# Kernel optimization log

Measured on AMD Instinct MI355X. Metric: run time of the kernel, lower is better.

The kernel has to match this reference:

```python
import jax, jax.numpy as jnp
import numpy as np

BZ, N_STEPS, D_IN, D_HID, D_OUT = 4096, 128, 32, 128, 32


def setup_inputs() -> dict:
    key = jax.random.key(0)
    ks = jax.random.split(key, 16)
    g = lambda k, s: jax.random.normal(k, s, dtype=jnp.float32) * 0.05
    return {
        "fcn_latent": g(ks[0], (BZ, D_IN)),
        "encoder_outputs": g(ks[1], (BZ, N_STEPS, D_HID)),
        "att1_w": g(ks[2], (D_IN, 2 * D_IN)),
        "att1_b": g(ks[3], (D_IN,)),
        "att2_w": g(ks[4], (D_HID, 2 * D_HID)),
        "att2_b": g(ks[5], (D_HID,)),
        "gru1_wih": g(ks[6], (3 * D_HID, D_IN)),
        "gru1_whh": g(ks[7], (3 * D_HID, D_HID)),
        "gru1_bih": g(ks[8], (3 * D_HID,)),
        "gru1_bhh": g(ks[9], (3 * D_HID,)),
        "gru2_wih": g(ks[10], (3 * D_HID, D_HID)),
        "gru2_whh": g(ks[11], (3 * D_HID, D_HID)),
        "gru2_bih": g(ks[12], (3 * D_HID,)),
        "gru2_bhh": g(ks[13], (3 * D_HID,)),
        "out_w": g(ks[14], (D_OUT, D_HID)),
        "out_b": g(ks[15], (D_OUT,)),
    }


def _gru_cell(x, h, w_ih, w_hh, b_ih, b_hh):
    # torch.nn.GRUCell math: gates ordered (r, z, n)
    gi = x @ w_ih.T + b_ih
    gh = h @ w_hh.T + b_hh
    i_r, i_z, i_n = jnp.split(gi, 3, axis=-1)
    h_r, h_z, h_n = jnp.split(gh, 3, axis=-1)
    r = jax.nn.sigmoid(i_r + h_r)
    z = jax.nn.sigmoid(i_z + h_z)
    n = jnp.tanh(i_n + r * h_n)
    return (1.0 - z) * n + z * h


def _attend(h, enc_t, w, b):
    # h: (bz, D), enc_t: (bz, d_enc). Faithful to original (mixes batch into contraction).
    scores = h.T @ enc_t                     # (D, d_enc)
    weight = jax.nn.softmax(scores, axis=-1)
    context = (weight @ enc_t.T).T           # (bz, D)
    return jnp.tanh(jnp.concatenate([context, h], axis=1) @ w.T + b)


def reference(fcn_latent, encoder_outputs, att1_w, att1_b, att2_w, att2_b,
              gru1_wih, gru1_whh, gru1_bih, gru1_bhh,
              gru2_wih, gru2_whh, gru2_bih, gru2_bhh, out_w, out_b):
    # step 0: attention over d_input-sized hidden, then GRUCell(d_input -> d_hidden)
    att0 = _attend(fcn_latent, encoder_outputs[:, 0, :], att1_w, att1_b)
    h_rep = jnp.tile(fcn_latent, (1, D_HID // D_IN))          # (bz, d_hidden)
    h = _gru_cell(att0, h_rep, gru1_wih, gru1_whh, gru1_bih, gru1_bhh)

    def step(h, enc_t):
        a = _attend(h, enc_t, att2_w, att2_b)
        h2 = _gru_cell(a, h, gru2_wih, gru2_whh, gru2_bih, gru2_bhh)
        return h2, h2

    enc_rest = jnp.swapaxes(encoder_outputs[:, 1:, :], 0, 1)  # (n_steps-1, bz, d_hidden)
    _, hs_rest = jax.lax.scan(step, h, enc_rest)
    collector = jnp.concatenate([h[:, None, :], jnp.swapaxes(hs_rest, 0, 1)], axis=1)
    reconstruction = collector @ out_w.T + out_b              # (bz, n_steps, d_output)
    return reconstruction
```

## Files before the change

### kernel.cpp

```cpp
#include <hip/hip_runtime.h>
#include <math.h>

#define BZ 4096
#define NT 128
#define DH 128
#define DI 32
#define LDW 132
#define SCR_KS 2116
#define SA 136
#define ST 40

typedef short bf16x8 __attribute__((ext_vector_type(8)));
typedef float f32x4 __attribute__((ext_vector_type(4)));

__device__ __forceinline__ float4 ld4(const float* p) { return *(const float4*)(p); }
__device__ __forceinline__ void st4(float* p, float4 v) { *(float4*)(p) = v; }
__device__ __forceinline__ float dot4(float4 w, float4 a) {
  return w.x*a.x + w.y*a.y + w.z*a.z + w.w*a.w;
}
__device__ __forceinline__ float sigm(float x) { return 1.f / (1.f + expf(-x)); }
__device__ __forceinline__ unsigned short f2b(float x) {
  unsigned u = __float_as_uint(x);
  u += 0x7FFFu + ((u >> 16) & 1u);
  return (unsigned short)(u >> 16);
}

__global__ __launch_bounds__(512) void k_prep(const float* __restrict__ a2w,
                                              const float* __restrict__ wih,
                                              const float* __restrict__ whh,
                                              const float* __restrict__ outw,
                                              unsigned short* __restrict__ wbf) {
  const int idx = blockIdx.x * 512 + threadIdx.x;
  if (idx >= 147456) return;
  const int tile = idx >> 14, pos = idx & 16383;
  float v;
  if (tile == 0)      v = a2w[(pos >> 7) * 256 + (pos & 127)];
  else if (tile == 1) v = a2w[(pos >> 7) * 256 + 128 + (pos & 127)];
  else if (tile == 2) v = wih[pos];
  else if (tile == 3) v = whh[pos];
  else if (tile == 4) v = wih[16384 + pos];
  else if (tile == 5) v = whh[16384 + pos];
  else if (tile == 6) v = wih[32768 + pos];
  else if (tile == 7) v = whh[32768 + pos];
  else                v = (pos < 4096) ? outw[pos] : 0.f;
  wbf[idx] = f2b(v);
}

template<int D>
__global__ __launch_bounds__(512) void k_scores(const float* __restrict__ hsrc,
                                                const float* __restrict__ enc,
                                                int t, float* __restrict__ spart) {
  constexpr int IG = D / 8;
  constexpr int JC = (D == 128) ? 4 : 1;
  constexpr int HS = D + 4;
  __shared__ float hs[64 * HS];
  __shared__ float es[64 * LDW];
  const int p = blockIdx.x, tid = threadIdx.x, b0 = p * 64;
  for (int idx = tid; idx < 64 * (D / 4); idx += 512) {
    const int r = idx / (D / 4), c4 = (idx % (D / 4)) * 4;
    st4(hs + r * HS + c4, ld4(hsrc + (size_t)(b0 + r) * D + c4));
  }
  for (int idx = tid; idx < 64 * 32; idx += 512) {
    const int r = idx >> 5, c4 = (idx & 31) << 2;
    st4(es + r * LDW + c4, ld4(enc + ((size_t)(b0 + r) * NT + t) * DH + c4));
  }
  __syncthreads();
  const int ig = tid % IG, jg = tid / IG;
  const int i0 = ig * 8, j0 = jg * JC;
  float acc[8][JC];
#pragma unroll
  for (int a = 0; a < 8; ++a)
#pragma unroll
    for (int b = 0; b < JC; ++b) acc[a][b] = 0.f;
  for (int b = 0; b < 64; ++b) {
    float4 h0 = ld4(hs + b * HS + i0);
    float4 h1 = ld4(hs + b * HS + i0 + 4);
    float hv[8] = {h0.x, h0.y, h0.z, h0.w, h1.x, h1.y, h1.z, h1.w};
    float ev[JC];
    if (JC == 4) {
      float4 e = ld4(es + b * LDW + j0);
      ev[0] = e.x; ev[1] = e.y; ev[2] = e.z; ev[3] = e.w;
    } else {
      ev[0] = es[b * LDW + j0];
    }
#pragma unroll
    for (int ii = 0; ii < 8; ++ii)
#pragma unroll
      for (int jj = 0; jj < JC; ++jj) acc[ii][jj] += hv[ii] * ev[jj];
  }
#pragma unroll
  for (int ii = 0; ii < 8; ++ii)
#pragma unroll
    for (int jj = 0; jj < JC; ++jj)
      spart[((size_t)p * D + (i0 + ii)) * 128 + j0 + jj] = acc[ii][jj];
}

template<int R, int P>
__global__ __launch_bounds__(128) void k_soft(const float* __restrict__ spart,
                                              float* __restrict__ W,
                                              unsigned short* __restrict__ Wmb) {
  const int r = blockIdx.x, j = threadIdx.x;
  float s = 0.f;
#pragma unroll 8
  for (int p = 0; p < P; ++p) s += spart[((size_t)p * R + r) * 128 + j];
  __shared__ float xm[2], xs[2];
  float m = s;
  for (int o = 1; o < 64; o <<= 1) m = fmaxf(m, __shfl_xor(m, o));
  if ((j & 63) == 0) xm[j >> 6] = m;
  __syncthreads();
  m = fmaxf(xm[0], xm[1]);
  float e = expf(s - m);
  float sum = e;
  for (int o = 1; o < 64; o <<= 1) sum += __shfl_xor(sum, o);
  if ((j & 63) == 0) xs[j >> 6] = sum;
  __syncthreads();
  sum = xs[0] + xs[1];
  const float val = e / sum;
  W[r * 128 + j] = val;
  Wmb[r * 128 + j] = f2b(val);
}

__global__ __launch_bounds__(128) void k_sum(const float* __restrict__ spart,
                                             float* __restrict__ S1,
                                             float* __restrict__ S2) {
  const int r = blockIdx.x, j = threadIdx.x;
  float s = 0.f;
#pragma unroll 8
  for (int p = 0; p < 64; ++p) s += spart[((size_t)p * 128 + r) * 128 + j];
  S1[r * 128 + j] = s;
  S2[r * 128 + j] = 0.f;
}

struct WTile { bf16x8 k[4]; };
struct AFrag { bf16x8 k[4]; };

__device__ __forceinline__ void loadW(WTile& wt, const unsigned short* __restrict__ base,
                                      int R, int g) {
#pragma unroll
  for (int ks = 0; ks < 4; ++ks)
    wt.k[ks] = *(const bf16x8*)(base + (size_t)R * 128 + ks * 32 + g * 8);
}
__device__ __forceinline__ void loadA(AFrag& a, const unsigned short* act, int n, int g) {
  const char* ab = (const char*)act + n * (2 * SA) + g * 16;
#pragma unroll
  for (int ks = 0; ks < 4; ++ks) a.k[ks] = *(const bf16x8*)(ab + ks * 64);
}
__device__ __forceinline__ void mmrr(f32x4& acc, const AFrag& a, const WTile& w) {
#pragma unroll
  for (int ks = 0; ks < 4; ++ks)
    acc = __builtin_amdgcn_mfma_f32_16x16x32_bf16(a.k[ks], w.k[ks], acc, 0, 0, 0);
}
__device__ __forceinline__ void mmls(f32x4& acc, const unsigned short* Wt,
                                     const unsigned short* act, int R, int n, int g) {
  const char* ab = (const char*)act + n * (2 * SA) + g * 16;
  const char* wb = (const char*)Wt;
  const int sw = (R & 7) << 4;
#pragma unroll
  for (int ks = 0; ks < 4; ++ks) {
    bf16x8 b = *(const bf16x8*)(wb + ((R * 256 + ks * 64 + g * 16) ^ sw));
    bf16x8 a = *(const bf16x8*)(ab + ks * 64);
    acc = __builtin_amdgcn_mfma_f32_16x16x32_bf16(a, b, acc, 0, 0, 0);
  }
}

__global__ __launch_bounds__(512, 2) void k_step3(
    const float* __restrict__ enc, int t, int do_next,
    const float* __restrict__ Srd, float* __restrict__ Sac, float* __restrict__ Szr,
    const unsigned short* __restrict__ wbf,
    const float* __restrict__ att2b,
    const float* __restrict__ bih, const float* __restrict__ bhh,
    const float* __restrict__ outb,
    float* __restrict__ h, float* __restrict__ out) {
  __shared__ __align__(16) unsigned short Wslot[16384];
  __shared__ __align__(16) unsigned short el[32 * SA], hl[32 * SA];
  __shared__ __align__(16) unsigned short ctxl[32 * SA], al[32 * SA], hnl[32 * SA];
  __shared__ __align__(16) unsigned short hnT[128 * ST], encT[128 * ST];
  const int tid = threadIdx.x, b0 = blockIdx.x * 32;
  const int w = tid >> 6, l = tid & 63;
  const int n = l & 15, g4 = l >> 4;
  const int c = w * 16 + n;
  const f32x4 z4 = {0.f, 0.f, 0.f, 0.f};

  {
    const int row = tid >> 2, q = tid & 3;
    const float* sr = Srd + row * 128 + q * 32;
    float4 v[8];
    float mx = -1e30f;
#pragma unroll
    for (int i = 0; i < 8; ++i) {
      v[i] = ld4(sr + 4 * i);
      mx = fmaxf(mx, fmaxf(fmaxf(v[i].x, v[i].y), fmaxf(v[i].z, v[i].w)));
    }
    mx = fmaxf(mx, __shfl_xor(mx, 1));
    mx = fmaxf(mx, __shfl_xor(mx, 2));
    float sum = 0.f;
#pragma unroll
    for (int i = 0; i < 8; ++i) {
      v[i].x = expf(v[i].x - mx); v[i].y = expf(v[i].y - mx);
      v[i].z = expf(v[i].z - mx); v[i].w = expf(v[i].w - mx);
      sum += (v[i].x + v[i].y) + (v[i].z + v[i].w);
    }
    sum += __shfl_xor(sum, 1);
    sum += __shfl_xor(sum, 2);
    const float inv = 1.f / sum;
    char* wb = (char*)Wslot;
    const int sw = (row & 7) << 4;
#pragma unroll
    for (int ch = 0; ch < 4; ++ch) {
      unsigned short h8[8] = {
        f2b(v[2*ch].x * inv),   f2b(v[2*ch].y * inv),
        f2b(v[2*ch].z * inv),   f2b(v[2*ch].w * inv),
        f2b(v[2*ch+1].x * inv), f2b(v[2*ch+1].y * inv),
        f2b(v[2*ch+1].z * inv), f2b(v[2*ch+1].w * inv)
      };
      *(uint4*)(wb + ((row * 256 + q * 64 + ch * 16) ^ sw)) = *(const uint4*)h8;
    }
  }

  {
    const int r = tid >> 4, c8 = (tid & 15) << 3;
    float4 e0 = ld4(enc + ((size_t)(b0 + r) * NT + t) * DH + c8);
    float4 e1 = ld4(enc + ((size_t)(b0 + r) * NT + t) * DH + c8 + 4);
    float4 h0 = ld4(h + (size_t)(b0 + r) * DH + c8);
    float4 h1 = ld4(h + (size_t)(b0 + r) * DH + c8 + 4);
    unsigned short e8[8] = {f2b(e0.x), f2b(e0.y), f2b(e0.z), f2b(e0.w),
                            f2b(e1.x), f2b(e1.y), f2b(e1.z), f2b(e1.w)};
    unsigned short h8[8] = {f2b(h0.x), f2b(h0.y), f2b(h0.z), f2b(h0.w),
                            f2b(h1.x), f2b(h1.y), f2b(h1.z), f2b(h1.w)};
    *(uint4*)(el + r * SA + c8) = *(const uint4*)e8;
    *(uint4*)(hl + r * SA + c8) = *(const uint4*)h8;
  }
  if (do_next) {
    const int r = tid & 31, c8 = (tid >> 5) << 3;
    float4 e0 = ld4(enc + ((size_t)(b0 + r) * NT + t + 1) * DH + c8);
    float4 e1 = ld4(enc + ((size_t)(b0 + r) * NT + t + 1) * DH + c8 + 4);
    encT[(c8 + 0) * ST + r] = f2b(e0.x); encT[(c8 + 1) * ST + r] = f2b(e0.y);
    encT[(c8 + 2) * ST + r] = f2b(e0.z); encT[(c8 + 3) * ST + r] = f2b(e0.w);
    encT[(c8 + 4) * ST + r] = f2b(e1.x); encT[(c8 + 5) * ST + r] = f2b(e1.y);
    encT[(c8 + 6) * ST + r] = f2b(e1.z); encT[(c8 + 7) * ST + r] = f2b(e1.w);
  }
  if (do_next && tid < 128) Szr[blockIdx.x * 128 + tid] = 0.f;

  WTile wA2a, wA2b, wIR, wHR, wIZ, wHZ, wIN, wHN;
  loadW(wA2a, wbf + 0 * 16384, c, g4);
  loadW(wA2b, wbf + 1 * 16384, c, g4);
  loadW(wIR,  wbf + 2 * 16384, c, g4);
  loadW(wHR,  wbf + 3 * 16384, c, g4);
  loadW(wIZ,  wbf + 4 * 16384, c, g4);
  loadW(wHZ,  wbf + 5 * 16384, c, g4);
  loadW(wIN,  wbf + 6 * 16384, c, g4);
  loadW(wHN,  wbf + 7 * 16384, c, g4);

  float hprev[2][4];
#pragma unroll
  for (int hh = 0; hh < 2; ++hh)
#pragma unroll
    for (int j = 0; j < 4; ++j)
      hprev[hh][j] = h[(size_t)(b0 + hh * 16 + g4 * 4 + j) * DH + c];
  const float b2c = att2b[c];
  const float bihR = bih[c], bihZ = bih[DH + c], bihN = bih[2 * DH + c];
  const float bhhR = bhh[c], bhhZ = bhh[DH + c], bhhN = bhh[2 * DH + c];
  __syncthreads();

#pragma unroll
  for (int hh = 0; hh < 2; ++hh) {
    f32x4 aC = z4;
    mmls(aC, Wslot, el + hh * 16 * SA, c, n, g4);
#pragma unroll
    for (int j = 0; j < 4; ++j) ctxl[(hh * 16 + g4 * 4 + j) * SA + c] = f2b(aC[j]);
  }
  __syncthreads();
#pragma unroll
  for (int hh = 0; hh < 2; ++hh) {
    AFrag fC, fH;
    loadA(fC, ctxl + hh * 16 * SA, n, g4);
    loadA(fH, hl + hh * 16 * SA, n, g4);
    f32x4 aA = z4;
    mmrr(aA, fC, wA2a);
    mmrr(aA, fH, wA2b);
#pragma unroll
    for (int j = 0; j < 4; ++j)
      al[(hh * 16 + g4 * 4 + j) * SA + c] = f2b(tanhf(aA[j] + b2c));
  }
  __syncthreads();
  f32x4 aR[2], aZ[2], aIN[2], aHN[2];
#pragma unroll
  for (int hh = 0; hh < 2; ++hh) {
    AFrag fA, fH;
    loadA(fA, al + hh * 16 * SA, n, g4);
    loadA(fH, hl + hh * 16 * SA, n, g4);
    f32x4 tr_ = z4, tz = z4, ti = z4, th = z4;
    mmrr(tr_, fA, wIR); mmrr(tr_, fH, wHR);
    mmrr(tz, fA, wIZ);  mmrr(tz, fH, wHZ);
    mmrr(ti, fA, wIN);  mmrr(th, fH, wHN);
    aR[hh] = tr_; aZ[hh] = tz; aIN[hh] = ti; aHN[hh] = th;
  }
#pragma unroll
  for (int hh = 0; hh < 2; ++hh) {
#pragma unroll
    for (int j = 0; j < 4; ++j) {
      const int row = hh * 16 + g4 * 4 + j;
      const float rg = sigm(aR[hh][j] + bihR + bhhR);
      const float zg = sigm(aZ[hh][j] + bihZ + bhhZ);
      const float ng = tanhf(aIN[hh][j] + bihN + rg * (aHN[hh][j] + bhhN));
      const float hv = (1.f - zg) * ng + zg * hprev[hh][j];
      const unsigned short hb = f2b(hv);
      hnl[row * SA + c] = hb;
      hnT[c * ST + row] = hb;
      h[(size_t)(b0 + row) * DH + c] = hv;
    }
  }
  __syncthreads();
  if (w < 2) {
    WTile wOut;
    loadW(wOut, wbf + 8 * 16384, c, g4);
    const float ob = outb[c];
#pragma unroll
    for (int hh = 0; hh < 2; ++hh) {
      AFrag fO;
      loadA(fO, hnl + hh * 16 * SA, n, g4);
      f32x4 o = z4;
      mmrr(o, fO, wOut);
#pragma unroll
      for (int j = 0; j < 4; ++j)
        out[((size_t)(b0 + hh * 16 + g4 * 4 + j) * NT + t) * DI + c] = o[j] + ob;
    }
  }
  if (do_next) {
    bf16x8 afr = *(const bf16x8*)(hnT + (16 * w + n) * ST + g4 * 8);
    float* Sn = Sac + (size_t)(16 * w + g4 * 4) * 128 + n;
#pragma unroll
    for (int nt = 0; nt < 8; ++nt) {
      bf16x8 bfr = *(const bf16x8*)(encT + (16 * nt + n) * ST + g4 * 8);
      f32x4 s = __builtin_amdgcn_mfma_f32_16x16x32_bf16(afr, bfr, z4, 0, 0, 0);
#pragma unroll
      for (int jj = 0; jj < 4; ++jj) atomicAdd(Sn + jj * 128 + nt * 16, s[jj]);
    }
  }
}

__device__ __forceinline__ void stage128(float* dst, const float* __restrict__ src,
                                         int rows, int srcStride, int tid) {
  const int n4 = rows * 32;
  for (int idx = tid; idx < n4; idx += 512) {
    const int r = idx >> 5, c4 = (idx & 31) << 2;
    st4(dst + r * LDW + c4, ld4(src + (size_t)r * srcStride + c4));
  }
}
template<int ADD>
__device__ __forceinline__ void phase128(float* Wb, const float* act, float* dest, int tid) {
  const int ks = tid & 7, cg_ = (tid >> 3) & 15, r4 = tid >> 7;
  const int rbase = r4 * 4;
  float acc[4][8];
#pragma unroll
  for (int a = 0; a < 4; ++a)
#pragma unroll
    for (int b = 0; b < 8; ++b) acc[a][b] = 0.f;
#pragma unroll
  for (int ch = 0; ch < 4; ++ch) {
    const int k = ks * 4 + ch * 32;
    float4 av[4];
#pragma unroll
    for (int ri = 0; ri < 4; ++ri) av[ri] = ld4(act + (rbase + ri) * LDW + k);
#pragma unroll
    for (int i = 0; i < 8; ++i) {
      float4 wv = ld4(Wb + (cg_ * 8 + i) * LDW + k);
#pragma unroll
      for (int ri = 0; ri < 4; ++ri) acc[ri][i] += dot4(wv, av[ri]);
    }
  }
  __syncthreads();
#pragma unroll
  for (int ri = 0; ri < 4; ++ri) {
    st4(Wb + ks * SCR_KS + (rbase + ri) * LDW + cg_ * 8,
        make_float4(acc[ri][0], acc[ri][1], acc[ri][2], acc[ri][3]));
    st4(Wb + ks * SCR_KS + (rbase + ri) * LDW + cg_ * 8 + 4,
        make_float4(acc[ri][4], acc[ri][5], acc[ri][6], acc[ri][7]));
  }
  __syncthreads();
  const int fr = tid >> 5, fc = (tid & 31) << 2;
  float4 s = make_float4(0.f, 0.f, 0.f, 0.f);
#pragma unroll
  for (int kk = 0; kk < 8; ++kk) {
    float4 v = ld4(Wb + kk * SCR_KS + fr * LDW + fc);
    s.x += v.x; s.y += v.y; s.z += v.z; s.w += v.w;
  }
  float* dp = dest + fr * LDW + fc;
  if (ADD) { float4 o = ld4(dp); s.x += o.x; s.y += o.y; s.z += o.z; s.w += o.w; }
  st4(dp, s);
  __syncthreads();
}
__device__ __forceinline__ void gru_out(float p0, float p1, float p2, float p3,
                                        float bi0, float bi1, float bi2,
                                        float bh0, float bh1, float bh2,
                                        float hv, float* o) {
  const float rg = sigm(p0 + bi0 + bh0);
  const float zg = sigm(p1 + bi1 + bh1);
  const float ng = tanhf(p2 + bi2 + rg * (p3 + bh2));
  *o = (1.f - zg) * ng + zg * hv;
}
__global__ __launch_bounds__(512) void k_main0(
    const float* __restrict__ enc, const float* __restrict__ fcn,
    const float* __restrict__ W0,
    const float* __restrict__ A1, const float* __restrict__ b1,
    const float* __restrict__ wih, const float* __restrict__ whh,
    const float* __restrict__ bih, const float* __restrict__ bhh,
    const float* __restrict__ outw, const float* __restrict__ outb,
    float* __restrict__ h, float* __restrict__ out) {
  __shared__ float Wb[16960];
  __shared__ float el[16 * LDW], hrep[16 * LDW], al[16 * LDW], hn[16 * LDW];
  __shared__ float pre[4][16 * LDW];
  __shared__ float fl[16 * 36];
  const int tid = threadIdx.x, b0 = blockIdx.x * 16;
  {
    const int r = tid >> 5, c4 = (tid & 31) << 2;
    st4(el + r * LDW + c4, ld4(enc + ((size_t)(b0 + r) * NT + 0) * DH + c4));
  }
  {
    const int r = tid >> 5, cc = tid & 31;
    fl[r * 36 + cc] = fcn[(size_t)(b0 + r) * DI + cc];
  }
  __syncthreads();
  {
    const int r = tid >> 5, fc = (tid & 31) << 2;
    st4(hrep + r * LDW + fc, ld4(fl + r * 36 + (fc & 31)));
  }
  stage128(Wb, W0, 32, 128, tid);
  __syncthreads();
  {
    const int r = tid >> 5, q = tid & 31;
    float acc = 0.f;
#pragma unroll 8
    for (int k4 = 0; k4 < 32; ++k4)
      acc += dot4(ld4(Wb + q * LDW + k4 * 4), ld4(el + r * LDW + k4 * 4));
    hn[r * LDW + q] = acc;
  }
  __syncthreads();
  for (int idx = tid; idx < 512; idx += 512) {
    const int r = idx >> 4, c4 = (idx & 15) << 2;
    st4(Wb + r * 68 + c4, ld4(A1 + r * 64 + c4));
  }
  __syncthreads();
  {
    const int r = tid >> 5, i = tid & 31;
    float acc = b1[i];
#pragma unroll
    for (int k4 = 0; k4 < 8; ++k4)
      acc += dot4(ld4(Wb + i * 68 + k4 * 4), ld4(hn + r * LDW + k4 * 4));
#pragma unroll
    for (int k4 = 0; k4 < 8; ++k4)
      acc += dot4(ld4(Wb + i * 68 + 32 + k4 * 4), ld4(fl + r * 36 + k4 * 4));
    al[r * LDW + i] = tanhf(acc);
  }
  __syncthreads();
  for (int idx = tid; idx < 384 * 8; idx += 512) {
    const int r = idx >> 3, c4 = (idx & 7) << 2;
    st4(Wb + r * 36 + c4, ld4(wih + r * 32 + c4));
  }
  __syncthreads();
  {
    const int r = tid >> 5, ccc = tid & 31;
#pragma unroll
    for (int m = 0; m < 12; ++m) {
      const int cc = ccc + 32 * m, g = cc >> 7, col = cc & 127;
      float acc = 0.f;
#pragma unroll
      for (int k4 = 0; k4 < 8; ++k4)
        acc += dot4(ld4(Wb + cc * 36 + k4 * 4), ld4(al + r * LDW + k4 * 4));
      pre[(g == 2) ? 2 : g][r * LDW + col] = acc;
    }
  }
  __syncthreads();
  stage128(Wb, whh, 128, 128, tid);          __syncthreads();
  phase128<1>(Wb, hrep, pre[0], tid);
  stage128(Wb, whh + 16384, 128, 128, tid);  __syncthreads();
  phase128<1>(Wb, hrep, pre[1], tid);
  stage128(Wb, whh + 32768, 128, 128, tid);  __syncthreads();
  phase128<0>(Wb, hrep, pre[3], tid);
  {
    const int fr = tid >> 5, fc = (tid & 31) << 2;
    float4 p0 = ld4(&pre[0][fr * LDW + fc]), p1 = ld4(&pre[1][fr * LDW + fc]);
    float4 p2 = ld4(&pre[2][fr * LDW + fc]), p3 = ld4(&pre[3][fr * LDW + fc]);
    float4 bi0 = ld4(bih + fc), bi1 = ld4(bih + DH + fc), bi2 = ld4(bih + 2 * DH + fc);
    float4 bh0 = ld4(bhh + fc), bh1 = ld4(bhh + DH + fc), bh2 = ld4(bhh + 2 * DH + fc);
    float4 hv = ld4(hrep + fr * LDW + fc);
    float o0, o1, o2, o3;
    gru_out(p0.x, p1.x, p2.x, p3.x, bi0.x, bi1.x, bi2.x, bh0.x, bh1.x, bh2.x, hv.x, &o0);
    gru_out(p0.y, p1.y, p2.y, p3.y, bi0.y, bi1.y, bi2.y, bh0.y, bh1.y, bh2.y, hv.y, &o1);
    gru_out(p0.z, p1.z, p2.z, p3.z, bi0.z, bi1.z, bi2.z, bh0.z, bh1.z, bh2.z, hv.z, &o2);
    gru_out(p0.w, p1.w, p2.w, p3.w, bi0.w, bi1.w, bi2.w, bh0.w, bh1.w, bh2.w, hv.w, &o3);
    float4 hnew = make_float4(o0, o1, o2, o3);
    st4(hn + fr * LDW + fc, hnew);
    st4(h + (size_t)(b0 + fr) * DH + fc, hnew);
  }
  __syncthreads();
  stage128(Wb, outw, 32, 128, tid);
  __syncthreads();
  {
    const int r = tid >> 5, cc = tid & 31;
    float acc = outb[cc];
#pragma unroll 8
    for (int k4 = 0; k4 < 32; ++k4)
      acc += dot4(ld4(Wb + cc * LDW + k4 * 4), ld4(hn + r * LDW + k4 * 4));
    out[((size_t)(b0 + r) * NT + 0) * DI + cc] = acc;
  }
}

extern "C" void kernel_launch(void* const* d_in, const int* in_sizes, int n_in,
                              void* d_out, int out_size, void* d_ws, size_t ws_size,
                              hipStream_t stream) {
  (void)in_sizes; (void)n_in; (void)out_size; (void)ws_size;
  const float* fcn  = (const float*)d_in[0];
  const float* enc  = (const float*)d_in[1];
  const float* a1w  = (const float*)d_in[2];
  const float* a1b  = (const float*)d_in[3];
  const float* a2w  = (const float*)d_in[4];
  const float* a2b  = (const float*)d_in[5];
  const float* w1ih = (const float*)d_in[6];
  const float* w1hh = (const float*)d_in[7];
  const float* b1ih = (const float*)d_in[8];
  const float* b1hh = (const float*)d_in[9];
  const float* w2ih = (const float*)d_in[10];
  const float* w2hh = (const float*)d_in[11];
  const float* b2ih = (const float*)d_in[12];
  const float* b2hh = (const float*)d_in[13];
  const float* outw = (const float*)d_in[14];
  const float* outb = (const float*)d_in[15];
  float* out = (float*)d_out;
  float* ws  = (float*)d_ws;

  float* h     = ws;
  float* spart = ws + 524288;
  float* Wbuf  = ws + 1572864;
  float* Sbuf  = ws + 1589248;
  unsigned short* wbf = (unsigned short*)(ws + 1654784);
  unsigned short* Wmb = (unsigned short*)(ws + 1728512);

  k_prep<<<288, 512, 0, stream>>>(a2w, w2ih, w2hh, outw, wbf);

  k_scores<DI><<<64, 512, 0, stream>>>(fcn, enc, 0, spart);
  k_soft<DI, 64><<<DI, 128, 0, stream>>>(spart, Wbuf, Wmb);
  k_main0<<<BZ / 16, 512, 0, stream>>>(enc, fcn, Wbuf, a1w, a1b,
                                       w1ih, w1hh, b1ih, b1hh, outw, outb, h, out);
  k_scores<DH><<<64, 512, 0, stream>>>(h, enc, 1, spart);
  k_sum<<<128, 128, 0, stream>>>(spart, Sbuf + 16384, Sbuf + 2 * 16384);

  for (int t = 1; t < NT; ++t) {
    const int do_next = (t < NT - 1) ? 1 : 0;
    const float* Srd = Sbuf + (size_t)(t & 3) * 16384;
    float* Sac = Sbuf + (size_t)((t + 1) & 3) * 16384;
    float* Szr = Sbuf + (size_t)((t + 2) & 3) * 16384;
    k_step3<<<128, 512, 0, stream>>>(enc, t, do_next, Srd, Sac, Szr, wbf, a2b,
                                     b2ih, b2hh, outb, h, out);
  }
}
```

Measured before the change: 3.242 ms.

## Halve per-block batch rows and keep softmax weights in registers

```diff
diff --git a/kernel.cpp b/kernel.cpp
--- a/kernel.cpp
+++ b/kernel.cpp
@@ -8,7 +8,7 @@
 #define LDW 132
 #define SCR_KS 2116
 #define SA 136
-#define ST 40
+#define ST2 48
 
 typedef short bf16x8 __attribute__((ext_vector_type(8)));
 typedef float f32x4 __attribute__((ext_vector_type(4)));
@@ -150,20 +150,8 @@
   for (int ks = 0; ks < 4; ++ks)
     acc = __builtin_amdgcn_mfma_f32_16x16x32_bf16(a.k[ks], w.k[ks], acc, 0, 0, 0);
 }
-__device__ __forceinline__ void mmls(f32x4& acc, const unsigned short* Wt,
-                                     const unsigned short* act, int R, int n, int g) {
-  const char* ab = (const char*)act + n * (2 * SA) + g * 16;
-  const char* wb = (const char*)Wt;
-  const int sw = (R & 7) << 4;
-#pragma unroll
-  for (int ks = 0; ks < 4; ++ks) {
-    bf16x8 b = *(const bf16x8*)(wb + ((R * 256 + ks * 64 + g * 16) ^ sw));
-    bf16x8 a = *(const bf16x8*)(ab + ks * 64);
-    acc = __builtin_amdgcn_mfma_f32_16x16x32_bf16(a, b, acc, 0, 0, 0);
-  }
-}
-
-__global__ __launch_bounds__(512, 2) void k_step3(
+
+__global__ __launch_bounds__(512, 2) void k_step4(
     const float* __restrict__ enc, int t, int do_next,
     const float* __restrict__ Srd, float* __restrict__ Sac, float* __restrict__ Szr,
     const unsigned short* __restrict__ wbf,
@@ -171,28 +159,29 @@
     const float* __restrict__ bih, const float* __restrict__ bhh,
     const float* __restrict__ outb,
     float* __restrict__ h, float* __restrict__ out) {
-  __shared__ __align__(16) unsigned short Wslot[16384];
-  __shared__ __align__(16) unsigned short el[32 * SA], hl[32 * SA];
-  __shared__ __align__(16) unsigned short ctxl[32 * SA], al[32 * SA], hnl[32 * SA];
-  __shared__ __align__(16) unsigned short hnT[128 * ST], encT[128 * ST];
-  const int tid = threadIdx.x, b0 = blockIdx.x * 32;
+  __shared__ __align__(16) unsigned short el[16 * SA], hl[16 * SA];
+  __shared__ __align__(16) unsigned short ctxl[16 * SA], al[16 * SA], hnl[16 * SA];
+  __shared__ __align__(16) unsigned short hnT[128 * ST2], encT[128 * ST2];
+  const int tid = threadIdx.x, b0 = blockIdx.x * 16;
   const int w = tid >> 6, l = tid & 63;
   const int n = l & 15, g4 = l >> 4;
   const int c = w * 16 + n;
   const f32x4 z4 = {0.f, 0.f, 0.f, 0.f};
 
-  {
-    const int row = tid >> 2, q = tid & 3;
-    const float* sr = Srd + row * 128 + q * 32;
+  WTile wW;
+  {
+    const float* sr = Srd + c * 128 + g4 * 8;
     float4 v[8];
     float mx = -1e30f;
 #pragma unroll
-    for (int i = 0; i < 8; ++i) {
-      v[i] = ld4(sr + 4 * i);
-      mx = fmaxf(mx, fmaxf(fmaxf(v[i].x, v[i].y), fmaxf(v[i].z, v[i].w)));
-    }
-    mx = fmaxf(mx, __shfl_xor(mx, 1));
-    mx = fmaxf(mx, __shfl_xor(mx, 2));
+    for (int ks = 0; ks < 4; ++ks) {
+      v[2 * ks]     = ld4(sr + ks * 32);
+      v[2 * ks + 1] = ld4(sr + ks * 32 + 4);
+      mx = fmaxf(mx, fmaxf(fmaxf(v[2*ks].x, v[2*ks].y), fmaxf(v[2*ks].z, v[2*ks].w)));
+      mx = fmaxf(mx, fmaxf(fmaxf(v[2*ks+1].x, v[2*ks+1].y), fmaxf(v[2*ks+1].z, v[2*ks+1].w)));
+    }
+    mx = fmaxf(mx, __shfl_xor(mx, 16));
+    mx = fmaxf(mx, __shfl_xor(mx, 32));
     float sum = 0.f;
 #pragma unroll
     for (int i = 0; i < 8; ++i) {
@@ -200,24 +189,22 @@
       v[i].z = expf(v[i].z - mx); v[i].w = expf(v[i].w - mx);
       sum += (v[i].x + v[i].y) + (v[i].z + v[i].w);
     }
-    sum += __shfl_xor(sum, 1);
-    sum += __shfl_xor(sum, 2);
+    sum += __shfl_xor(sum, 16);
+    sum += __shfl_xor(sum, 32);
     const float inv = 1.f / sum;
-    char* wb = (char*)Wslot;
-    const int sw = (row & 7) << 4;
-#pragma unroll
-    for (int ch = 0; ch < 4; ++ch) {
+#pragma unroll
+    for (int ks = 0; ks < 4; ++ks) {
       unsigned short h8[8] = {
-        f2b(v[2*ch].x * inv),   f2b(v[2*ch].y * inv),
-        f2b(v[2*ch].z * inv),   f2b(v[2*ch].w * inv),
-        f2b(v[2*ch+1].x * inv), f2b(v[2*ch+1].y * inv),
-        f2b(v[2*ch+1].z * inv), f2b(v[2*ch+1].w * inv)
+        f2b(v[2*ks].x * inv),   f2b(v[2*ks].y * inv),
+        f2b(v[2*ks].z * inv),   f2b(v[2*ks].w * inv),
+        f2b(v[2*ks+1].x * inv), f2b(v[2*ks+1].y * inv),
+        f2b(v[2*ks+1].z * inv), f2b(v[2*ks+1].w * inv)
       };
-      *(uint4*)(wb + ((row * 256 + q * 64 + ch * 16) ^ sw)) = *(const uint4*)h8;
-    }
-  }
-
-  {
+      wW.k[ks] = *(const bf16x8*)h8;
+    }
+  }
+
+  if (tid < 256) {
     const int r = tid >> 4, c8 = (tid & 15) << 3;
     float4 e0 = ld4(enc + ((size_t)(b0 + r) * NT + t) * DH + c8);
     float4 e1 = ld4(enc + ((size_t)(b0 + r) * NT + t) * DH + c8 + 4);
@@ -229,109 +216,103 @@
                             f2b(h1.x), f2b(h1.y), f2b(h1.z), f2b(h1.w)};
     *(uint4*)(el + r * SA + c8) = *(const uint4*)e8;
     *(uint4*)(hl + r * SA + c8) = *(const uint4*)h8;
-  }
-  if (do_next) {
-    const int r = tid & 31, c8 = (tid >> 5) << 3;
+  } else if (do_next) {
+    const int idx = tid - 256;
+    const int r = idx & 15, c8 = (idx >> 4) << 3;
     float4 e0 = ld4(enc + ((size_t)(b0 + r) * NT + t + 1) * DH + c8);
     float4 e1 = ld4(enc + ((size_t)(b0 + r) * NT + t + 1) * DH + c8 + 4);
-    encT[(c8 + 0) * ST + r] = f2b(e0.x); encT[(c8 + 1) * ST + r] = f2b(e0.y);
-    encT[(c8 + 2) * ST + r] = f2b(e0.z); encT[(c8 + 3) * ST + r] = f2b(e0.w);
-    encT[(c8 + 4) * ST + r] = f2b(e1.x); encT[(c8 + 5) * ST + r] = f2b(e1.y);
-    encT[(c8 + 6) * ST + r] = f2b(e1.z); encT[(c8 + 7) * ST + r] = f2b(e1.w);
-  }
-  if (do_next && tid < 128) Szr[blockIdx.x * 128 + tid] = 0.f;
-
-  WTile wA2a, wA2b, wIR, wHR, wIZ, wHZ, wIN, wHN;
-  loadW(wA2a, wbf + 0 * 16384, c, g4);
-  loadW(wA2b, wbf + 1 * 16384, c, g4);
-  loadW(wIR,  wbf + 2 * 16384, c, g4);
-  loadW(wHR,  wbf + 3 * 16384, c, g4);
-  loadW(wIZ,  wbf + 4 * 16384, c, g4);
-  loadW(wHZ,  wbf + 5 * 16384, c, g4);
-  loadW(wIN,  wbf + 6 * 16384, c, g4);
-  loadW(wHN,  wbf + 7 * 16384, c, g4);
-
-  float hprev[2][4];
-#pragma unroll
-  for (int hh = 0; hh < 2; ++hh)
-#pragma unroll
-    for (int j = 0; j < 4; ++j)
-      hprev[hh][j] = h[(size_t)(b0 + hh * 16 + g4 * 4 + j) * DH + c];
+    encT[(c8 + 0) * ST2 + r] = f2b(e0.x); encT[(c8 + 1) * ST2 + r] = f2b(e0.y);
+    encT[(c8 + 2) * ST2 + r] = f2b(e0.z); encT[(c8 + 3) * ST2 + r] = f2b(e0.w);
+    encT[(c8 + 4) * ST2 + r] = f2b(e1.x); encT[(c8 + 5) * ST2 + r] = f2b(e1.y);
+    encT[(c8 + 6) * ST2 + r] = f2b(e1.z); encT[(c8 + 7) * ST2 + r] = f2b(e1.w);
+  }
+  if (do_next) {
+    for (int q = tid; q < 128 * 32; q += 512) {
+      const int col = q >> 5, p = q & 31;
+      hnT[col * ST2 + 16 + p] = 0;
+      encT[col * ST2 + 16 + p] = 0;
+    }
+    if (tid < 64) Szr[blockIdx.x * 64 + tid] = 0.f;
+  }
+
+  float hprev[4];
+#pragma unroll
+  for (int j = 0; j < 4; ++j)
+    hprev[j] = h[(size_t)(b0 + g4 * 4 + j) * DH + c];
   const float b2c = att2b[c];
   const float bihR = bih[c], bihZ = bih[DH + c], bihN = bih[2 * DH + c];
   const float bhhR = bhh[c], bhhZ = bhh[DH + c], bhhN = bhh[2 * DH + c];
-  __syncthreads();
-
-#pragma unroll
-  for (int hh = 0; hh < 2; ++hh) {
+
+  WTile wA, wB;
+  loadW(wA, wbf + 0 * 16384, c, g4);
+  loadW(wB, wbf + 1 * 16384, c, g4);
+  __syncthreads();
+
+  {
+    AFrag fE;
+    loadA(fE, el, n, g4);
     f32x4 aC = z4;
-    mmls(aC, Wslot, el + hh * 16 * SA, c, n, g4);
-#pragma unroll
-    for (int j = 0; j < 4; ++j) ctxl[(hh * 16 + g4 * 4 + j) * SA + c] = f2b(aC[j]);
-  }
-  __syncthreads();
-#pragma unroll
-  for (int hh = 0; hh < 2; ++hh) {
-    AFrag fC, fH;
-    loadA(fC, ctxl + hh * 16 * SA, n, g4);
-    loadA(fH, hl + hh * 16 * SA, n, g4);
+    mmrr(aC, fE, wW);
+#pragma unroll
+    for (int j = 0; j < 4; ++j) ctxl[(g4 * 4 + j) * SA + c] = f2b(aC[j]);
+  }
+  __syncthreads();
+  AFrag fH;
+  loadA(fH, hl, n, g4);
+  {
+    AFrag fC;
+    loadA(fC, ctxl, n, g4);
     f32x4 aA = z4;
-    mmrr(aA, fC, wA2a);
-    mmrr(aA, fH, wA2b);
+    mmrr(aA, fC, wA);
+    mmrr(aA, fH, wB);
 #pragma unroll
     for (int j = 0; j < 4; ++j)
-      al[(hh * 16 + g4 * 4 + j) * SA + c] = f2b(tanhf(aA[j] + b2c));
-  }
-  __syncthreads();
-  f32x4 aR[2], aZ[2], aIN[2], aHN[2];
-#pragma unroll
-  for (int hh = 0; hh < 2; ++hh) {
-    AFrag fA, fH;
-    loadA(fA, al + hh * 16 * SA, n, g4);
-    loadA(fH, hl + hh * 16 * SA, n, g4);
-    f32x4 tr_ = z4, tz = z4, ti = z4, th = z4;
-    mmrr(tr_, fA, wIR); mmrr(tr_, fH, wHR);
-    mmrr(tz, fA, wIZ);  mmrr(tz, fH, wHZ);
-    mmrr(ti, fA, wIN);  mmrr(th, fH, wHN);
-    aR[hh] = tr_; aZ[hh] = tz; aIN[hh] = ti; aHN[hh] = th;
-  }
-#pragma unroll
-  for (int hh = 0; hh < 2; ++hh) {
-#pragma unroll
-    for (int j = 0; j < 4; ++j) {
-      const int row = hh * 16 + g4 * 4 + j;
-      const float rg = sigm(aR[hh][j] + bihR + bhhR);
-      const float zg = sigm(aZ[hh][j] + bihZ + bhhZ);
-      const float ng = tanhf(aIN[hh][j] + bihN + rg * (aHN[hh][j] + bhhN));
-      const float hv = (1.f - zg) * ng + zg * hprev[hh][j];
-      const unsigned short hb = f2b(hv);
-      hnl[row * SA + c] = hb;
-      hnT[c * ST + row] = hb;
-      h[(size_t)(b0 + row) * DH + c] = hv;
-    }
+      al[(g4 * 4 + j) * SA + c] = f2b(tanhf(aA[j] + b2c));
+  }
+  loadW(wA, wbf + 2 * 16384, c, g4);
+  loadW(wB, wbf + 3 * 16384, c, g4);
+  __syncthreads();
+  AFrag fA;
+  loadA(fA, al, n, g4);
+  f32x4 aR = z4, aZ = z4, aIN = z4, aHN = z4;
+  mmrr(aR, fA, wA); mmrr(aR, fH, wB);
+  loadW(wA, wbf + 4 * 16384, c, g4);
+  loadW(wB, wbf + 5 * 16384, c, g4);
+  mmrr(aZ, fA, wA); mmrr(aZ, fH, wB);
+  loadW(wA, wbf + 6 * 16384, c, g4);
+  loadW(wB, wbf + 7 * 16384, c, g4);
+  mmrr(aIN, fA, wA); mmrr(aHN, fH, wB);
+#pragma unroll
+  for (int j = 0; j < 4; ++j) {
+    const int row = g4 * 4 + j;
+    const float rg = sigm(aR[j] + bihR + bhhR);
+    const float zg = sigm(aZ[j] + bihZ + bhhZ);
+    const float ng = tanhf(aIN[j] + bihN + rg * (aHN[j] + bhhN));
+    const float hv = (1.f - zg) * ng + zg * hprev[j];
+    const unsigned short hb = f2b(hv);
+    hnl[row * SA + c] = hb;
+    hnT[c * ST2 + row] = hb;
+    h[(size_t)(b0 + row) * DH + c] = hv;
   }
   __syncthreads();
   if (w < 2) {
     WTile wOut;
     loadW(wOut, wbf + 8 * 16384, c, g4);
+    AFrag fO;
+    loadA(fO, hnl, n, g4);
+    f32x4 o = z4;
+    mmrr(o, fO, wOut);
     const float ob = outb[c];
 #pragma unroll
-    for (int hh = 0; hh < 2; ++hh) {
-      AFrag fO;
-      loadA(fO, hnl + hh * 16 * SA, n, g4);
-      f32x4 o = z4;
-      mmrr(o, fO, wOut);
-#pragma unroll
-      for (int j = 0; j < 4; ++j)
-        out[((size_t)(b0 + hh * 16 + g4 * 4 + j) * NT + t) * DI + c] = o[j] + ob;
-    }
+    for (int j = 0; j < 4; ++j)
+      out[((size_t)(b0 + g4 * 4 + j) * NT + t) * DI + c] = o[j] + ob;
   }
   if (do_next) {
-    bf16x8 afr = *(const bf16x8*)(hnT + (16 * w + n) * ST + g4 * 8);
+    bf16x8 afr = *(const bf16x8*)(hnT + (16 * w + n) * ST2 + g4 * 8);
     float* Sn = Sac + (size_t)(16 * w + g4 * 4) * 128 + n;
 #pragma unroll
     for (int nt = 0; nt < 8; ++nt) {
-      bf16x8 bfr = *(const bf16x8*)(encT + (16 * nt + n) * ST + g4 * 8);
+      bf16x8 bfr = *(const bf16x8*)(encT + (16 * nt + n) * ST2 + g4 * 8);
       f32x4 s = __builtin_amdgcn_mfma_f32_16x16x32_bf16(afr, bfr, z4, 0, 0, 0);
 #pragma unroll
       for (int jj = 0; jj < 4; ++jj) atomicAdd(Sn + jj * 128 + nt * 16, s[jj]);
@@ -550,7 +531,7 @@
     const float* Srd = Sbuf + (size_t)(t & 3) * 16384;
     float* Sac = Sbuf + (size_t)((t + 1) & 3) * 16384;
     float* Szr = Sbuf + (size_t)((t + 2) & 3) * 16384;
-    k_step3<<<128, 512, 0, stream>>>(enc, t, do_next, Srd, Sac, Szr, wbf, a2b,
+    k_step4<<<256, 512, 0, stream>>>(enc, t, do_next, Srd, Sac, Szr, wbf, a2b,
                                      b2ih, b2hh, outb, h, out);
   }
 }
```

Result: slower. 4.099 ms (+26.5%).

## Defer output projection to a batched kernel over stored hidden-state history

Applied to the files above, without the earlier changes.

```diff
diff --git a/kernel.cpp b/kernel.cpp
--- a/kernel.cpp
+++ b/kernel.cpp
@@ -169,17 +169,18 @@
     const unsigned short* __restrict__ wbf,
     const float* __restrict__ att2b,
     const float* __restrict__ bih, const float* __restrict__ bhh,
-    const float* __restrict__ outb,
-    float* __restrict__ h, float* __restrict__ out) {
+    float* __restrict__ hist) {
   __shared__ __align__(16) unsigned short Wslot[16384];
   __shared__ __align__(16) unsigned short el[32 * SA], hl[32 * SA];
-  __shared__ __align__(16) unsigned short ctxl[32 * SA], al[32 * SA], hnl[32 * SA];
+  __shared__ __align__(16) unsigned short ctxl[32 * SA], al[32 * SA];
   __shared__ __align__(16) unsigned short hnT[128 * ST], encT[128 * ST];
   const int tid = threadIdx.x, b0 = blockIdx.x * 32;
   const int w = tid >> 6, l = tid & 63;
   const int n = l & 15, g4 = l >> 4;
   const int c = w * 16 + n;
   const f32x4 z4 = {0.f, 0.f, 0.f, 0.f};
+  const float* __restrict__ hprev_g = hist + (size_t)(t - 1) * (BZ * DH);
+  float* __restrict__ hcur_g = hist + (size_t)t * (BZ * DH);
 
   {
     const int row = tid >> 2, q = tid & 3;
@@ -221,8 +222,8 @@
     const int r = tid >> 4, c8 = (tid & 15) << 3;
     float4 e0 = ld4(enc + ((size_t)(b0 + r) * NT + t) * DH + c8);
     float4 e1 = ld4(enc + ((size_t)(b0 + r) * NT + t) * DH + c8 + 4);
-    float4 h0 = ld4(h + (size_t)(b0 + r) * DH + c8);
-    float4 h1 = ld4(h + (size_t)(b0 + r) * DH + c8 + 4);
+    float4 h0 = ld4(hprev_g + (size_t)(b0 + r) * DH + c8);
+    float4 h1 = ld4(hprev_g + (size_t)(b0 + r) * DH + c8 + 4);
     unsigned short e8[8] = {f2b(e0.x), f2b(e0.y), f2b(e0.z), f2b(e0.w),
                             f2b(e1.x), f2b(e1.y), f2b(e1.z), f2b(e1.w)};
     unsigned short h8[8] = {f2b(h0.x), f2b(h0.y), f2b(h0.z), f2b(h0.w),
@@ -256,7 +257,7 @@
   for (int hh = 0; hh < 2; ++hh)
 #pragma unroll
     for (int j = 0; j < 4; ++j)
-      hprev[hh][j] = h[(size_t)(b0 + hh * 16 + g4 * 4 + j) * DH + c];
+      hprev[hh][j] = hprev_g[(size_t)(b0 + hh * 16 + g4 * 4 + j) * DH + c];
   const float b2c = att2b[c];
   const float bihR = bih[c], bihZ = bih[DH + c], bihN = bih[2 * DH + c];
   const float bhhR = bhh[c], bhhZ = bhh[DH + c], bhhN = bhh[2 * DH + c];
@@ -304,29 +305,13 @@
       const float zg = sigm(aZ[hh][j] + bihZ + bhhZ);
       const float ng = tanhf(aIN[hh][j] + bihN + rg * (aHN[hh][j] + bhhN));
       const float hv = (1.f - zg) * ng + zg * hprev[hh][j];
-      const unsigned short hb = f2b(hv);
-      hnl[row * SA + c] = hb;
-      hnT[c * ST + row] = hb;
-      h[(size_t)(b0 + row) * DH + c] = hv;
-    }
-  }
-  __syncthreads();
-  if (w < 2) {
-    WTile wOut;
-    loadW(wOut, wbf + 8 * 16384, c, g4);
-    const float ob = outb[c];
-#pragma unroll
-    for (int hh = 0; hh < 2; ++hh) {
-      AFrag fO;
-      loadA(fO, hnl + hh * 16 * SA, n, g4);
-      f32x4 o = z4;
-      mmrr(o, fO, wOut);
-#pragma unroll
-      for (int j = 0; j < 4; ++j)
-        out[((size_t)(b0 + hh * 16 + g4 * 4 + j) * NT + t) * DI + c] = o[j] + ob;
-    }
-  }
-  if (do_next) {
+      hnT[c * ST + row] = f2b(hv);
+      hcur_g[(size_t)(b0 + row) * DH + c] = hv;
+    }
+  }
+  if (!do_next) return;
+  __syncthreads();
+  {
     bf16x8 afr = *(const bf16x8*)(hnT + (16 * w + n) * ST + g4 * 8);
     float* Sn = Sac + (size_t)(16 * w + g4 * 4) * 128 + n;
 #pragma unroll
@@ -336,6 +321,48 @@
 #pragma unroll
       for (int jj = 0; jj < 4; ++jj) atomicAdd(Sn + jj * 128 + nt * 16, s[jj]);
     }
+  }
+}
+
+__global__ __launch_bounds__(256) void k_out(const float* __restrict__ hist,
+                                             const float* __restrict__ outw,
+                                             const float* __restrict__ outb,
+                                             float* __restrict__ out) {
+  __shared__ float wl[32 * 132];
+  __shared__ float bl[32];
+  const int tid = threadIdx.x;
+  for (int idx = tid; idx < 32 * 32; idx += 256) {
+    const int r = idx >> 5, c4 = (idx & 31) << 2;
+    st4(wl + r * 132 + c4, ld4(outw + r * 128 + c4));
+  }
+  if (tid < 32) bl[tid] = outb[tid];
+  __syncthreads();
+  const int rlocal = tid >> 2, q = tid & 3;
+  const size_t ri = (size_t)blockIdx.x * 64 + rlocal;
+  const int b = (int)(ri & 4095), t = 1 + (int)(ri >> 12);
+  const float* hr = hist + (size_t)t * (BZ * DH) + (size_t)b * DH + q * 32;
+  float4 hv[8];
+#pragma unroll
+  for (int i = 0; i < 8; ++i) hv[i] = ld4(hr + 4 * i);
+  float acc[32];
+#pragma unroll
+  for (int o = 0; o < 32; ++o) {
+    const float* wr = wl + o * 132 + q * 32;
+    float a = 0.f;
+#pragma unroll
+    for (int i = 0; i < 8; ++i) a += dot4(ld4(wr + 4 * i), hv[i]);
+    acc[o] = a;
+  }
+#pragma unroll
+  for (int o = 0; o < 32; ++o) {
+    acc[o] += __shfl_xor(acc[o], 1);
+    acc[o] += __shfl_xor(acc[o], 2);
+  }
+  float* op = out + ((size_t)b * NT + t) * DI;
+#pragma unroll
+  for (int oo = 0; oo < 8; ++oo) {
+    const int o = q * 8 + oo;
+    op[o] = acc[o] + bl[o];
   }
 }
 
@@ -529,20 +556,20 @@
   float* out = (float*)d_out;
   float* ws  = (float*)d_ws;
 
-  float* h     = ws;
-  float* spart = ws + 524288;
-  float* Wbuf  = ws + 1572864;
-  float* Sbuf  = ws + 1589248;
-  unsigned short* wbf = (unsigned short*)(ws + 1654784);
-  unsigned short* Wmb = (unsigned short*)(ws + 1728512);
+  float* spart = ws;
+  float* Wbuf  = ws + 1048576;
+  float* Sbuf  = ws + 1064960;
+  unsigned short* wbf = (unsigned short*)(ws + 1130496);
+  unsigned short* Wmb = (unsigned short*)(ws + 1204224);
+  float* hist  = ws + 1310720;
 
   k_prep<<<288, 512, 0, stream>>>(a2w, w2ih, w2hh, outw, wbf);
 
   k_scores<DI><<<64, 512, 0, stream>>>(fcn, enc, 0, spart);
   k_soft<DI, 64><<<DI, 128, 0, stream>>>(spart, Wbuf, Wmb);
   k_main0<<<BZ / 16, 512, 0, stream>>>(enc, fcn, Wbuf, a1w, a1b,
-                                       w1ih, w1hh, b1ih, b1hh, outw, outb, h, out);
-  k_scores<DH><<<64, 512, 0, stream>>>(h, enc, 1, spart);
+                                       w1ih, w1hh, b1ih, b1hh, outw, outb, hist, out);
+  k_scores<DH><<<64, 512, 0, stream>>>(hist, enc, 1, spart);
   k_sum<<<128, 128, 0, stream>>>(spart, Sbuf + 16384, Sbuf + 2 * 16384);
 
   for (int t = 1; t < NT; ++t) {
@@ -551,6 +578,7 @@
     float* Sac = Sbuf + (size_t)((t + 1) & 3) * 16384;
     float* Szr = Sbuf + (size_t)((t + 2) & 3) * 16384;
     k_step3<<<128, 512, 0, stream>>>(enc, t, do_next, Srd, Sac, Szr, wbf, a2b,
-                                     b2ih, b2hh, outb, h, out);
-  }
-}
+                                     b2ih, b2hh, hist);
+  }
+  k_out<<<(BZ * (NT - 1)) / 64, 256, 0, stream>>>(hist, outw, outb, out);
+}
```

New measurement: 3.246 ms. No clear change (+0.1%).
